# Kernel tuning notes

Hardware: AMD Instinct MI355X
Metric: run time of the kernel (lower is better)

## Reference

```python
import jax, jax.numpy as jnp
import numpy as np

N = 40000
E = 640000
IN_C = 128
HID = 256
HEADS = 8


def _gat(x, W, att_src, att_dst, bias, src, dst, num_nodes, heads, concat):
    # x: [N, Fin], W: [Fin, heads*C], att_*: [heads, C], bias: [out_dim]
    xp = (x @ W).reshape(num_nodes, heads, -1)          # [N, H, C]
    a_s = jnp.sum(xp * att_src, axis=-1)                # [N, H]
    a_d = jnp.sum(xp * att_dst, axis=-1)                # [N, H]
    e = jax.nn.leaky_relu(a_s[src] + a_d[dst], 0.2)     # [E, H]
    # per-destination-node softmax over incoming edges (self-loops guarantee >=1)
    m = jax.ops.segment_max(e, dst, num_segments=num_nodes)
    m = jnp.where(jnp.isfinite(m), m, 0.0)
    ex = jnp.exp(e - m[dst])
    denom = jax.ops.segment_sum(ex, dst, num_segments=num_nodes)
    alpha = ex / (denom[dst] + 1e-16)                   # [E, H]
    out = jax.ops.segment_sum(xp[src] * alpha[..., None], dst, num_segments=num_nodes)  # [N,H,C]
    out = out.reshape(num_nodes, -1) if concat else out.mean(axis=1)
    return out + bias


def setup_inputs() -> dict:
    key = jax.random.key(0)
    ks = jax.random.split(key, 16)
    C = HID // HEADS
    s = 0.05
    return {
        "x": jax.random.normal(ks[0], (N, IN_C), jnp.float32),
        "edge_index": jax.random.randint(ks[1], (2, E), 0, N, jnp.int32),
        "W0": jax.random.normal(ks[2], (IN_C, HEADS * C), jnp.float32) * s,
        "att_s0": jax.random.normal(ks[3], (HEADS, C), jnp.float32) * s,
        "att_d0": jax.random.normal(ks[4], (HEADS, C), jnp.float32) * s,
        "b0": jnp.zeros((HID,), jnp.float32),
        # BatchNorm(256)
        "gamma0": jnp.ones((HID,), jnp.float32),
        "beta0": jnp.zeros((HID,), jnp.float32),
        # skip projection Linear(128 -> 256)
        "W_skip": jax.random.normal(ks[5], (IN_C, HID), jnp.float32) * s,
        "b_skip": jnp.zeros((HID,), jnp.float32),
        # last layer: GATConv(256 -> 256, heads=1, concat=False)
        "W1": jax.random.normal(ks[6], (HID, HID), jnp.float32) * s,
        "att_s1": jax.random.normal(ks[7], (1, HID), jnp.float32) * s,
        "att_d1": jax.random.normal(ks[8], (1, HID), jnp.float32) * s,
        "b1": jnp.zeros((HID,), jnp.float32),
    }


def reference(x, edge_index, W0, att_s0, att_d0, b0, gamma0, beta0,
              W_skip, b_skip, W1, att_s1, att_d1, b1):
    loops = jnp.arange(N, dtype=edge_index.dtype)
    src = jnp.concatenate([edge_index[0], loops])
    dst = jnp.concatenate([edge_index[1], loops])
    # conv 0 (heads=8, concat)
    h = _gat(x, W0, att_s0, att_d0, b0, src, dst, N, HEADS, True)
    # BatchNorm (training-style batch stats, biased variance, eps=1e-5)
    mu = h.mean(axis=0)
    var = h.var(axis=0)
    h = (h - mu) / jnp.sqrt(var + 1e-5) * gamma0 + beta0
    h = jax.nn.elu(h)
    # dropout is identity in eval mode
    # residual: shapes differ (128 vs 256) -> skip_proj(x_initial) + h at i==0
    h = h + (x @ W_skip + b_skip)
    # conv 1 (heads=1, concat=False -> mean over single head)
    out = _gat(h, W1, att_s1, att_d1, b1, src, dst, N, 1, False)
    return out
```

## Files before the change

### kernel.cpp

```cpp
#include <hip/hip_runtime.h>
#include <hip/hip_bf16.h>

#define NN 40000
#define EE 640000
#define ET 680000
#define MPAD 40064
#define LOG2E 1.4426950408889634f

#define XN (MPAD * 128 / 4)
#define WN 131072
#define VN 512
#define PREP_TOTAL (XN + WN + VN + ET)

typedef __attribute__((ext_vector_type(8))) short short8;
typedef __attribute__((ext_vector_type(4))) float f32x4;

__device__ __forceinline__ float bf2f(unsigned u) {
    return __uint_as_float(u << 16);
}
__device__ __forceinline__ unsigned short f2bf(float f) {
    unsigned u = __float_as_uint(f);
    return (unsigned short)((u + 0x7FFFu + ((u >> 16) & 1u)) >> 16);
}
__device__ __forceinline__ unsigned pack2(float lo, float hi) {
    return ((unsigned)f2bf(lo)) | (((unsigned)f2bf(hi)) << 16);
}
__device__ __forceinline__ void unpack2(unsigned u, float& lo, float& hi) {
    lo = __uint_as_float(u << 16);
    hi = __uint_as_float(u & 0xffff0000u);
}

__global__ __launch_bounds__(256) void prep(
    const float* __restrict__ x, const float* __restrict__ W0,
    const float* __restrict__ Ws, const float* __restrict__ W1,
    const float* __restrict__ as1, const float* __restrict__ ad1,
    const int* __restrict__ ei,
    unsigned short* __restrict__ xb, unsigned short* __restrict__ Wtc,
    unsigned short* __restrict__ W1t, float* __restrict__ v,
    int* __restrict__ deg, int* __restrict__ erank)
{
    int i = blockIdx.x * 256 + threadIdx.x;
    if (i < XN) {
        int row = (i * 4) >> 7;
        ushort4 o;
        if (row < NN) {
            float4 val = ((const float4*)x)[i];
            o.x = f2bf(val.x); o.y = f2bf(val.y); o.z = f2bf(val.z); o.w = f2bf(val.w);
        } else { o.x = o.y = o.z = o.w = 0; }
        ((ushort4*)xb)[i] = o;
    } else if (i < XN + WN) {
        int j = i - XN;
        if (j < 32768) {
            int c = j >> 7, k = j & 127;
            Wtc[j] = f2bf(W0[(size_t)k * 256 + c]);
        } else if (j < 65536) {
            int jj = j - 32768;
            int c = jj >> 7, k = jj & 127;
            Wtc[j] = f2bf(Ws[(size_t)k * 256 + c]);
        } else {
            int jj = j - 65536;
            int c = jj >> 8, k = jj & 255;
            W1t[jj] = f2bf(W1[(size_t)k * 256 + c]);
        }
    } else if (i < XN + WN + VN) {
        int j = i - XN - WN;
        int k = j >> 1, which = j & 1;
        const float* att = which ? ad1 : as1;
        float sum = 0.f;
        for (int c = 0; c < 256; c++)
            sum += W1[(size_t)k * 256 + c] * att[c];
        v[j] = sum * LOG2E;
    } else {
        int e = i - XN - WN - VN;
        if (e < ET) {
            int d = (e < EE) ? ei[EE + e] : (e - EE);
            erank[e] = atomicAdd(&deg[d], 1);
        }
    }
}

__global__ __launch_bounds__(1024) void exscan(
    const int* __restrict__ deg, int* __restrict__ rowptr)
{
    __shared__ int wsum[16];
    __shared__ int carry_s;
    int tid = threadIdx.x, lane = tid & 63, wid = tid >> 6;
    if (tid == 0) carry_s = 0;
    __syncthreads();
    for (int base = 0; base < NN; base += 1024) {
        int i = base + tid;
        int val = (i < NN) ? deg[i] : 0;
        int sc = val;
        #pragma unroll
        for (int off = 1; off < 64; off <<= 1) {
            int t = __shfl_up(sc, off);
            if (lane >= off) sc += t;
        }
        if (lane == 63) wsum[wid] = sc;
        __syncthreads();
        if (wid == 0 && lane < 16) {
            int t = wsum[lane];
            #pragma unroll
            for (int off = 1; off < 16; off <<= 1) {
                int u = __shfl_up(t, off);
                if (lane >= off) t += u;
            }
            wsum[lane] = t;
        }
        __syncthreads();
        int carry = carry_s;
        int wpre = wid ? wsum[wid - 1] : 0;
        int excl = carry + wpre + sc - val;
        if (i < NN) rowptr[i] = excl;
        __syncthreads();
        if (tid == 0) carry_s = carry + wsum[15];
    }
    if (tid == 0) rowptr[NN] = carry_s;
}

__global__ __launch_bounds__(256) void csr_fill(
    const int* __restrict__ ei, const int* __restrict__ rowptr,
    const int* __restrict__ erank, int* __restrict__ adj)
{
    int e = blockIdx.x * blockDim.x + threadIdx.x;
    if (e >= ET) return;
    int s, d;
    if (e < EE) { s = ei[e]; d = ei[EE + e]; } else { s = d = e - EE; }
    adj[rowptr[d] + erank[e]] = s;
}

__global__ __launch_bounds__(256) void gemm0(
    const unsigned short* __restrict__ A, const unsigned short* __restrict__ Btc,
    unsigned short* __restrict__ C0, unsigned short* __restrict__ C1)
{
    __shared__ unsigned short As[128 * 64];
    const int K = 128;
    int tid = threadIdx.x;
    int rb = blockIdx.x * 128, cb = blockIdx.y * 128;
    int lane = tid & 63, wid = tid >> 6;
    int wm = (wid >> 1) * 64, wn = (wid & 1) * 64;
    int lr = lane & 15, lk = lane >> 4;
    f32x4 acc[4][4] = {};
    for (int kb = 0; kb < K; kb += 64) {
        #pragma unroll
        for (int i = 0; i < 4; i++) {
            int flat = tid + i * 256;
            int r = flat >> 3, c8 = flat & 7;
            int4 vv = *(const int4*)(A + (size_t)(rb + r) * K + kb + c8 * 8);
            *(int4*)(&As[r * 64 + ((c8 ^ (r & 7)) * 8)]) = vv;
        }
        __syncthreads();
        #pragma unroll
        for (int kk = 0; kk < 2; kk++) {
            int kbase = kb + kk * 32 + lk * 8;
            short8 bfr[4], afr[4];
            #pragma unroll
            for (int n = 0; n < 4; n++)
                bfr[n] = *(const short8*)(Btc + (size_t)(cb + wn + n * 16 + lr) * K + kbase);
            #pragma unroll
            for (int m = 0; m < 4; m++) {
                int row = wm + m * 16 + lr;
                int kchunk = kk * 4 + lk;
                afr[m] = *(const short8*)(&As[row * 64 + ((kchunk ^ (row & 7)) * 8)]);
            }
            #pragma unroll
            for (int m = 0; m < 4; m++)
                #pragma unroll
                for (int n = 0; n < 4; n++)
                    acc[m][n] = __builtin_amdgcn_mfma_f32_16x16x32_bf16(afr[m], bfr[n], acc[m][n], 0, 0, 0);
        }
        __syncthreads();
    }
    unsigned short* C = (cb < 256) ? C0 : C1;
    int cbase = cb & 255;
    #pragma unroll
    for (int m = 0; m < 4; m++)
        #pragma unroll
        for (int n = 0; n < 4; n++) {
            int col = cbase + wn + n * 16 + lr;
            #pragma unroll
            for (int j = 0; j < 4; j++) {
                int row = rb + wm + m * 16 + lk * 4 + j;
                C[(size_t)row * 256 + col] = f2bf(acc[m][n][j]);
            }
        }
}

__global__ __launch_bounds__(256) void gemm_bf16(
    const unsigned short* __restrict__ A, const unsigned short* __restrict__ Btc,
    unsigned short* __restrict__ C0, int K)
{
    __shared__ unsigned short As[128 * 64];
    int tid = threadIdx.x;
    int rb = blockIdx.x * 128, cb = blockIdx.y * 128;
    int lane = tid & 63, wid = tid >> 6;
    int wm = (wid >> 1) * 64, wn = (wid & 1) * 64;
    int lr = lane & 15, lk = lane >> 4;
    f32x4 acc[4][4] = {};
    for (int kb = 0; kb < K; kb += 64) {
        #pragma unroll
        for (int i = 0; i < 4; i++) {
            int flat = tid + i * 256;
            int r = flat >> 3, c8 = flat & 7;
            int4 vv = *(const int4*)(A + (size_t)(rb + r) * K + kb + c8 * 8);
            *(int4*)(&As[r * 64 + ((c8 ^ (r & 7)) * 8)]) = vv;
        }
        __syncthreads();
        #pragma unroll
        for (int kk = 0; kk < 2; kk++) {
            int kbase = kb + kk * 32 + lk * 8;
            short8 bfr[4], afr[4];
            #pragma unroll
            for (int n = 0; n < 4; n++)
                bfr[n] = *(const short8*)(Btc + (size_t)(cb + wn + n * 16 + lr) * K + kbase);
            #pragma unroll
            for (int m = 0; m < 4; m++) {
                int row = wm + m * 16 + lr;
                int kchunk = kk * 4 + lk;
                afr[m] = *(const short8*)(&As[row * 64 + ((kchunk ^ (row & 7)) * 8)]);
            }
            #pragma unroll
            for (int m = 0; m < 4; m++)
                #pragma unroll
                for (int n = 0; n < 4; n++)
                    acc[m][n] = __builtin_amdgcn_mfma_f32_16x16x32_bf16(afr[m], bfr[n], acc[m][n], 0, 0, 0);
        }
        __syncthreads();
    }
    #pragma unroll
    for (int m = 0; m < 4; m++)
        #pragma unroll
        for (int n = 0; n < 4; n++) {
            int col = cb + wn + n * 16 + lr;
            #pragma unroll
            for (int j = 0; j < 4; j++) {
                int row = rb + wm + m * 16 + lk * 4 + j;
                C0[(size_t)row * 256 + col] = f2bf(acc[m][n][j]);
            }
        }
}

__global__ __launch_bounds__(256) void attn_node0(
    const unsigned short* __restrict__ xp, const float* __restrict__ att_s,
    const float* __restrict__ att_d, float* __restrict__ a_s, float* __restrict__ a_d)
{
    int t = blockIdx.x * 256 + threadIdx.x;
    if (t >= NN * 8) return;
    int n = t >> 3, h = t & 7;
    const unsigned short* p = xp + (size_t)n * 256 + h * 32;
    float s = 0.f, dd = 0.f;
    #pragma unroll
    for (int i0 = 0; i0 < 32; i0 += 8) {
        uint4 raw = *(const uint4*)(p + i0);
        unsigned vals[4] = {raw.x, raw.y, raw.z, raw.w};
        #pragma unroll
        for (int q = 0; q < 4; q++) {
            float lo, hi;
            unpack2(vals[q], lo, hi);
            s  += lo * att_s[h * 32 + i0 + q * 2] + hi * att_s[h * 32 + i0 + q * 2 + 1];
            dd += lo * att_d[h * 32 + i0 + q * 2] + hi * att_d[h * 32 + i0 + q * 2 + 1];
        }
    }
    a_s[t] = s * LOG2E; a_d[t] = dd * LOG2E;
}

__global__ __launch_bounds__(256) void gather0(
    const int* __restrict__ adj, const int* __restrict__ rowptr,
    const unsigned short* __restrict__ xp, const float* __restrict__ a_s,
    const float* __restrict__ a_d, unsigned short* __restrict__ out0)
{
    int w = (blockIdx.x * 256 + threadIdx.x) >> 6;
    int lane = threadIdx.x & 63;
    if (w >= NN) return;
    int hl = lane & 31;
    int hw = lane >> 5;
    int h = hl >> 2;
    float ad = a_d[w * 8 + h];
    int p = rowptr[w], end = rowptr[w + 1];
    unsigned loff = (unsigned)hl * 16u;
    float a0=0,a1=0,a2=0,a3=0,a4=0,a5=0,a6=0,a7=0;
    float b0=0,b1=0,b2=0,b3=0,b4=0,b5=0,b6=0,b7=0;
    float den0 = 0.f, den1 = 0.f;
    float lo, hi;
    for (; p + 4 <= end; p += 4) {
        int sA = adj[p + hw];
        int sB = adj[p + 2 + hw];
        float eA = a_s[sA * 8 + h] + ad;
        float eB = a_s[sB * 8 + h] + ad;
        float wA = __builtin_amdgcn_exp2f(fmaxf(eA, 0.2f * eA));
        float wB = __builtin_amdgcn_exp2f(fmaxf(eB, 0.2f * eB));
        uint4 rA = *(const uint4*)((const char*)xp + ((unsigned)sA * 512u + loff));
        uint4 rB = *(const uint4*)((const char*)xp + ((unsigned)sB * 512u + loff));
        den0 += wA; den1 += wB;
        unpack2(rA.x, lo, hi); a0 += wA * lo; a1 += wA * hi;
        unpack2(rA.y, lo, hi); a2 += wA * lo; a3 += wA * hi;
        unpack2(rA.z, lo, hi); a4 += wA * lo; a5 += wA * hi;
        unpack2(rA.w, lo, hi); a6 += wA * lo; a7 += wA * hi;
        unpack2(rB.x, lo, hi); b0 += wB * lo; b1 += wB * hi;
        unpack2(rB.y, lo, hi); b2 += wB * lo; b3 += wB * hi;
        unpack2(rB.z, lo, hi); b4 += wB * lo; b5 += wB * hi;
        unpack2(rB.w, lo, hi); b6 += wB * lo; b7 += wB * hi;
    }
    for (; p + 2 <= end; p += 2) {
        int sA = adj[p + hw];
        float eA = a_s[sA * 8 + h] + ad;
        float wA = __builtin_amdgcn_exp2f(fmaxf(eA, 0.2f * eA));
        uint4 rA = *(const uint4*)((const char*)xp + ((unsigned)sA * 512u + loff));
        den0 += wA;
        unpack2(rA.x, lo, hi); a0 += wA * lo; a1 += wA * hi;
        unpack2(rA.y, lo, hi); a2 += wA * lo; a3 += wA * hi;
        unpack2(rA.z, lo, hi); a4 += wA * lo; a5 += wA * hi;
        unpack2(rA.w, lo, hi); a6 += wA * lo; a7 += wA * hi;
    }
    if (p < end) {
        int sA = adj[p];
        float eA = a_s[sA * 8 + h] + ad;
        float wA = hw ? 0.f : __builtin_amdgcn_exp2f(fmaxf(eA, 0.2f * eA));
        uint4 rA = *(const uint4*)((const char*)xp + ((unsigned)sA * 512u + loff));
        den0 += wA;
        unpack2(rA.x, lo, hi); a0 += wA * lo; a1 += wA * hi;
        unpack2(rA.y, lo, hi); a2 += wA * lo; a3 += wA * hi;
        unpack2(rA.z, lo, hi); a4 += wA * lo; a5 += wA * hi;
        unpack2(rA.w, lo, hi); a6 += wA * lo; a7 += wA * hi;
    }
    a0 += b0; a1 += b1; a2 += b2; a3 += b3;
    a4 += b4; a5 += b5; a6 += b6; a7 += b7;
    float den = den0 + den1;
    den += __shfl_xor(den, 32);
    a0 += __shfl_xor(a0, 32); a1 += __shfl_xor(a1, 32);
    a2 += __shfl_xor(a2, 32); a3 += __shfl_xor(a3, 32);
    a4 += __shfl_xor(a4, 32); a5 += __shfl_xor(a5, 32);
    a6 += __shfl_xor(a6, 32); a7 += __shfl_xor(a7, 32);
    if (hw == 0) {
        float inv = 1.f / (den + 1e-16f);
        uint4 o;
        o.x = pack2(a0 * inv, a1 * inv);
        o.y = pack2(a2 * inv, a3 * inv);
        o.z = pack2(a4 * inv, a5 * inv);
        o.w = pack2(a6 * inv, a7 * inv);
        *(uint4*)((char*)out0 + ((size_t)w * 512u + loff)) = o;
    }
}

__global__ __launch_bounds__(256) void bn_stats(
    const unsigned short* __restrict__ H, float* __restrict__ bnsum, float* __restrict__ bnsq)
{
    int c = threadIdx.x;
    int r0 = blockIdx.x * 64;
    float s = 0.f, sq = 0.f;
    for (int r = r0; r < r0 + 64; r++) {
        float val = bf2f(H[(size_t)r * 256 + c]);
        s += val; sq += val * val;
    }
    atomicAdd(&bnsum[c], s);
    atomicAdd(&bnsq[c], sq);
}

__global__ __launch_bounds__(256) void bn_elu_attn(
    const unsigned short* __restrict__ out0, unsigned short* __restrict__ hb,
    const float* __restrict__ bnsum, const float* __restrict__ bnsq,
    const float* __restrict__ gamma, const float* __restrict__ beta,
    const float* __restrict__ bskip, const float* __restrict__ v,
    float* __restrict__ a_s, float* __restrict__ a_d)
{
    int i = blockIdx.x * 256 + threadIdx.x;
    if (i >= MPAD * 32) return;
    int col0 = (i * 8) & 255;
    int row = i >> 5;
    uint4 hv = ((const uint4*)out0)[i];
    uint4 sv = ((const uint4*)hb)[i];
    float bn[8], sk[8];
    unpack2(hv.x, bn[0], bn[1]); unpack2(hv.y, bn[2], bn[3]);
    unpack2(hv.z, bn[4], bn[5]); unpack2(hv.w, bn[6], bn[7]);
    unpack2(sv.x, sk[0], sk[1]); unpack2(sv.y, sk[2], sk[3]);
    unpack2(sv.z, sk[4], sk[5]); unpack2(sv.w, sk[6], sk[7]);
    const float invN = 1.0f / (float)NN;
    float r[8];
    float ps = 0.f, pd = 0.f;
    #pragma unroll
    for (int q = 0; q < 8; q++) {
        int c = col0 + q;
        float mu = bnsum[c] * invN;
        float var = bnsq[c] * invN - mu * mu;
        float scl = rsqrtf(var + 1e-5f) * gamma[c];
        float b = (bn[q] - mu) * scl + beta[c];
        float el = b > 0.f ? b : (__expf(b) - 1.f);
        r[q] = el + sk[q] + bskip[c];
        float2 vv = *(const float2*)(v + c * 2);
        ps += r[q] * vv.x;
        pd += r[q] * vv.y;
    }
    uint4 o;
    o.x = pack2(r[0], r[1]); o.y = pack2(r[2], r[3]);
    o.z = pack2(r[4], r[5]); o.w = pack2(r[6], r[7]);
    ((uint4*)hb)[i] = o;
    #pragma unroll
    for (int off = 1; off < 32; off <<= 1) {
        ps += __shfl_xor(ps, off);
        pd += __shfl_xor(pd, off);
    }
    if ((threadIdx.x & 31) == 0 && row < NN) {
        a_s[row] = ps;
        a_d[row] = pd;
    }
}

__global__ __launch_bounds__(256) void gather1(
    const int* __restrict__ adj, const int* __restrict__ rowptr,
    const unsigned short* __restrict__ xp, const float* __restrict__ a_s,
    const float* __restrict__ a_d, const float* __restrict__ b1,
    float* __restrict__ out)
{
    int w = (blockIdx.x * 256 + threadIdx.x) >> 6;
    int lane = threadIdx.x & 63;
    if (w >= NN) return;
    int hl = lane & 31;
    int hw = lane >> 5;
    float ad = a_d[w];
    int p = rowptr[w], end = rowptr[w + 1];
    unsigned loff = (unsigned)hl * 16u;
    float a0=0,a1=0,a2=0,a3=0,a4=0,a5=0,a6=0,a7=0;
    float b0s=0,b1s=0,b2s=0,b3s=0,b4s=0,b5s=0,b6s=0,b7s=0;
    float den0 = 0.f, den1 = 0.f;
    float lo, hi;
    for (; p + 4 <= end; p += 4) {
        int sA = adj[p + hw];
        int sB = adj[p + 2 + hw];
        float eA = a_s[sA] + ad;
        float eB = a_s[sB] + ad;
        float wA = __builtin_amdgcn_exp2f(fmaxf(eA, 0.2f * eA));
        float wB = __builtin_amdgcn_exp2f(fmaxf(eB, 0.2f * eB));
        uint4 rA = *(const uint4*)((const char*)xp + ((unsigned)sA * 512u + loff));
        uint4 rB = *(const uint4*)((const char*)xp + ((unsigned)sB * 512u + loff));
        den0 += wA; den1 += wB;
        unpack2(rA.x, lo, hi); a0 += wA * lo; a1 += wA * hi;
        unpack2(rA.y, lo, hi); a2 += wA * lo; a3 += wA * hi;
        unpack2(rA.z, lo, hi); a4 += wA * lo; a5 += wA * hi;
        unpack2(rA.w, lo, hi); a6 += wA * lo; a7 += wA * hi;
        unpack2(rB.x, lo, hi); b0s += wB * lo; b1s += wB * hi;
        unpack2(rB.y, lo, hi); b2s += wB * lo; b3s += wB * hi;
        unpack2(rB.z, lo, hi); b4s += wB * lo; b5s += wB * hi;
        unpack2(rB.w, lo, hi); b6s += wB * lo; b7s += wB * hi;
    }
    for (; p + 2 <= end; p += 2) {
        int sA = adj[p + hw];
        float eA = a_s[sA] + ad;
        float wA = __builtin_amdgcn_exp2f(fmaxf(eA, 0.2f * eA));
        uint4 rA = *(const uint4*)((const char*)xp + ((unsigned)sA * 512u + loff));
        den0 += wA;
        unpack2(rA.x, lo, hi); a0 += wA * lo; a1 += wA * hi;
        unpack2(rA.y, lo, hi); a2 += wA * lo; a3 += wA * hi;
        unpack2(rA.z, lo, hi); a4 += wA * lo; a5 += wA * hi;
        unpack2(rA.w, lo, hi); a6 += wA * lo; a7 += wA * hi;
    }
    if (p < end) {
        int sA = adj[p];
        float eA = a_s[sA] + ad;
        float wA = hw ? 0.f : __builtin_amdgcn_exp2f(fmaxf(eA, 0.2f * eA));
        uint4 rA = *(const uint4*)((const char*)xp + ((unsigned)sA * 512u + loff));
        den0 += wA;
        unpack2(rA.x, lo, hi); a0 += wA * lo; a1 += wA * hi;
        unpack2(rA.y, lo, hi); a2 += wA * lo; a3 += wA * hi;
        unpack2(rA.z, lo, hi); a4 += wA * lo; a5 += wA * hi;
        unpack2(rA.w, lo, hi); a6 += wA * lo; a7 += wA * hi;
    }
    a0 += b0s; a1 += b1s; a2 += b2s; a3 += b3s;
    a4 += b4s; a5 += b5s; a6 += b6s; a7 += b7s;
    float den = den0 + den1;
    den += __shfl_xor(den, 32);
    a0 += __shfl_xor(a0, 32); a1 += __shfl_xor(a1, 32);
    a2 += __shfl_xor(a2, 32); a3 += __shfl_xor(a3, 32);
    a4 += __shfl_xor(a4, 32); a5 += __shfl_xor(a5, 32);
    a6 += __shfl_xor(a6, 32); a7 += __shfl_xor(a7, 32);
    if (hw == 0) {
        float inv = 1.f / (den + 1e-16f);
        const float* bb = b1 + hl * 8;
        float4 o0 = {a0 * inv + bb[0], a1 * inv + bb[1],
                     a2 * inv + bb[2], a3 * inv + bb[3]};
        float4 o1 = {a4 * inv + bb[4], a5 * inv + bb[5],
                     a6 * inv + bb[6], a7 * inv + bb[7]};
        float* orow = out + (size_t)w * 256 + hl * 8;
        *(float4*)(orow) = o0;
        *(float4*)(orow + 4) = o1;
    }
}

extern "C" void kernel_launch(void* const* d_in, const int* in_sizes, int n_in,
                              void* d_out, int out_size, void* d_ws, size_t ws_size,
                              hipStream_t stream)
{
    const float* x      = (const float*)d_in[0];
    const int*   ei     = (const int*)d_in[1];
    const float* W0     = (const float*)d_in[2];
    const float* att_s0 = (const float*)d_in[3];
    const float* att_d0 = (const float*)d_in[4];
    const float* gamma0 = (const float*)d_in[6];
    const float* beta0  = (const float*)d_in[7];
    const float* W_skip = (const float*)d_in[8];
    const float* b_skip = (const float*)d_in[9];
    const float* W1     = (const float*)d_in[10];
    const float* att_s1 = (const float*)d_in[11];
    const float* att_d1 = (const float*)d_in[12];
    const float* b1     = (const float*)d_in[13];
    float* out = (float*)d_out;

    char* p = (char*)d_ws;
    unsigned short* x_bf  = (unsigned short*)p; p += (size_t)MPAD * 128 * 2;
    unsigned short* xp_bf = (unsigned short*)p; p += (size_t)MPAD * 256 * 2;
    unsigned short* h_bf  = (unsigned short*)p; p += (size_t)MPAD * 256 * 2;
    unsigned short* out0b = (unsigned short*)p; p += (size_t)MPAD * 256 * 2;
    unsigned short* Wtc   = (unsigned short*)p; p += (size_t)512 * 128 * 2;
    unsigned short* W1t   = (unsigned short*)p; p += (size_t)256 * 256 * 2;
    float* v     = (float*)p; p += 512 * 4;
    float* a_s   = (float*)p; p += (size_t)NN * 8 * 4;
    float* a_d   = (float*)p; p += (size_t)NN * 8 * 4;
    int*   deg   = (int*)p;   p += (size_t)NN * 4;
    float* bnsum = (float*)p; p += 256 * 4;
    float* bnsq  = (float*)p; p += 256 * 4;
    int* rowptr = (int*)p; p += (size_t)(NN + 1) * 4;
    int* erank  = (int*)p; p += (size_t)ET * 4;
    int* adj    = (int*)p; p += (size_t)ET * 4;

    hipMemsetAsync(deg, 0, (size_t)(NN + 512) * 4, stream);
    hipMemsetAsync(out0b + (size_t)NN * 256, 0, (size_t)(MPAD - NN) * 256 * 2, stream);

    prep<<<(PREP_TOTAL + 255) / 256, 256, 0, stream>>>(
        x, W0, W_skip, W1, att_s1, att_d1, ei, x_bf, Wtc, W1t, v, deg, erank);

    exscan<<<1, 1024, 0, stream>>>(deg, rowptr);

    csr_fill<<<(ET + 255) / 256, 256, 0, stream>>>(ei, rowptr, erank, adj);

    dim3 gg0(MPAD / 128, 4);
    gemm0<<<gg0, 256, 0, stream>>>(x_bf, Wtc, xp_bf, h_bf);

    attn_node0<<<(NN * 8 + 255) / 256, 256, 0, stream>>>(xp_bf, att_s0, att_d0, a_s, a_d);

    gather0<<<(NN * 64 + 255) / 256, 256, 0, stream>>>(adj, rowptr, xp_bf, a_s, a_d, out0b);

    bn_stats<<<NN / 64, 256, 0, stream>>>(out0b, bnsum, bnsq);

    bn_elu_attn<<<(MPAD * 32 + 255) / 256, 256, 0, stream>>>(
        out0b, h_bf, bnsum, bnsq, gamma0, beta0, b_skip, v, a_s, a_d);

    dim3 gg1(MPAD / 128, 2);
    gemm_bf16<<<gg1, 256, 0, stream>>>(h_bf, W1t, xp_bf, 256);

    gather1<<<(NN * 64 + 255) / 256, 256, 0, stream>>>(adj, rowptr, xp_bf, a_s, a_d, b1, out);
}
```

Measured before the change: 288.6 us.

## Fold layer-0 attention vectors into W0 and merge attention with CSR fill

Precomputes u = W0·att (per head, scaled by log2e) in the prep kernel, so the layer-0 attention logits come straight from x in bf16 (128-wide dot products) rather than from the GEMM output. This removes the dependency on gemm0, which lets the attention computation join the CSR fill kernel and removes one launch. The tradeoff is more arithmetic per node (128 vs 32 elements per head), and the logits now differ slightly in rounding because they skip the bf16-rounded xp.

```diff
diff --git a/kernel.cpp b/kernel.cpp
--- a/kernel.cpp
+++ b/kernel.cpp
@@ -10,7 +10,11 @@
 #define XN (MPAD * 128 / 4)
 #define WN 131072
 #define VN 512
-#define PREP_TOTAL (XN + WN + VN + ET)
+#define UN 2048
+#define PREP_TOTAL (XN + WN + VN + UN + ET)
+
+#define FB ((ET + 255) / 256)
+#define AB ((NN * 8 + 255) / 256)
 
 typedef __attribute__((ext_vector_type(8))) short short8;
 typedef __attribute__((ext_vector_type(4))) float f32x4;
@@ -33,10 +37,11 @@
 __global__ __launch_bounds__(256) void prep(
     const float* __restrict__ x, const float* __restrict__ W0,
     const float* __restrict__ Ws, const float* __restrict__ W1,
+    const float* __restrict__ as0, const float* __restrict__ ad0,
     const float* __restrict__ as1, const float* __restrict__ ad1,
     const int* __restrict__ ei,
     unsigned short* __restrict__ xb, unsigned short* __restrict__ Wtc,
-    unsigned short* __restrict__ W1t, float* __restrict__ v,
+    unsigned short* __restrict__ W1t, float* __restrict__ v, float* __restrict__ u,
     int* __restrict__ deg, int* __restrict__ erank)
 {
     int i = blockIdx.x * 256 + threadIdx.x;
@@ -70,8 +75,18 @@
         for (int c = 0; c < 256; c++)
             sum += W1[(size_t)k * 256 + c] * att[c];
         v[j] = sum * LOG2E;
+    } else if (i < XN + WN + VN + UN) {
+        int j = i - XN - WN - VN;
+        int k = j >> 4, jj = j & 15;
+        int h = jj & 7;
+        const float* att = (jj < 8) ? as0 : ad0;
+        float sum = 0.f;
+        #pragma unroll
+        for (int c = 0; c < 32; c++)
+            sum += W0[(size_t)k * 256 + h * 32 + c] * att[h * 32 + c];
+        u[j] = sum * LOG2E;
     } else {
-        int e = i - XN - WN - VN;
+        int e = i - XN - WN - VN - UN;
         if (e < ET) {
             int d = (e < EE) ? ei[EE + e] : (e - EE);
             erank[e] = atomicAdd(&deg[d], 1);
@@ -102,8 +117,8 @@
             int t = wsum[lane];
             #pragma unroll
             for (int off = 1; off < 16; off <<= 1) {
-                int u = __shfl_up(t, off);
-                if (lane >= off) t += u;
+                int uu = __shfl_up(t, off);
+                if (lane >= off) t += uu;
             }
             wsum[lane] = t;
         }
@@ -118,15 +133,40 @@
     if (tid == 0) rowptr[NN] = carry_s;
 }
 
-__global__ __launch_bounds__(256) void csr_fill(
+__global__ __launch_bounds__(256) void fill_attn0(
     const int* __restrict__ ei, const int* __restrict__ rowptr,
-    const int* __restrict__ erank, int* __restrict__ adj)
-{
-    int e = blockIdx.x * blockDim.x + threadIdx.x;
-    if (e >= ET) return;
-    int s, d;
-    if (e < EE) { s = ei[e]; d = ei[EE + e]; } else { s = d = e - EE; }
-    adj[rowptr[d] + erank[e]] = s;
+    const int* __restrict__ erank, int* __restrict__ adj,
+    const unsigned short* __restrict__ xb, const float* __restrict__ u,
+    float* __restrict__ a_s, float* __restrict__ a_d)
+{
+    int tid = threadIdx.x;
+    if (blockIdx.x < FB) {
+        int e = blockIdx.x * 256 + tid;
+        if (e >= ET) return;
+        int s, d;
+        if (e < EE) { s = ei[e]; d = ei[EE + e]; } else { s = d = e - EE; }
+        adj[rowptr[d] + erank[e]] = s;
+        return;
+    }
+    int t = (blockIdx.x - FB) * 256 + tid;
+    if (t >= NN * 8) return;
+    int n = t >> 3, h = t & 7;
+    const uint4* xr = (const uint4*)(xb + (size_t)n * 128);
+    float s = 0.f, dd = 0.f;
+    #pragma unroll
+    for (int q = 0; q < 16; q++) {
+        uint4 raw = xr[q];
+        unsigned vals[4] = {raw.x, raw.y, raw.z, raw.w};
+        #pragma unroll
+        for (int r = 0; r < 4; r++) {
+            float lo, hi;
+            unpack2(vals[r], lo, hi);
+            int c = q * 8 + r * 2;
+            s  += lo * u[c * 16 + h]     + hi * u[(c + 1) * 16 + h];
+            dd += lo * u[c * 16 + 8 + h] + hi * u[(c + 1) * 16 + 8 + h];
+        }
+    }
+    a_s[t] = s; a_d[t] = dd;
 }
 
 __global__ __launch_bounds__(256) void gemm0(
@@ -238,30 +278,6 @@
                 C0[(size_t)row * 256 + col] = f2bf(acc[m][n][j]);
             }
         }
-}
-
-__global__ __launch_bounds__(256) void attn_node0(
-    const unsigned short* __restrict__ xp, const float* __restrict__ att_s,
-    const float* __restrict__ att_d, float* __restrict__ a_s, float* __restrict__ a_d)
-{
-    int t = blockIdx.x * 256 + threadIdx.x;
-    if (t >= NN * 8) return;
-    int n = t >> 3, h = t & 7;
-    const unsigned short* p = xp + (size_t)n * 256 + h * 32;
-    float s = 0.f, dd = 0.f;
-    #pragma unroll
-    for (int i0 = 0; i0 < 32; i0 += 8) {
-        uint4 raw = *(const uint4*)(p + i0);
-        unsigned vals[4] = {raw.x, raw.y, raw.z, raw.w};
-        #pragma unroll
-        for (int q = 0; q < 4; q++) {
-            float lo, hi;
-            unpack2(vals[q], lo, hi);
-            s  += lo * att_s[h * 32 + i0 + q * 2] + hi * att_s[h * 32 + i0 + q * 2 + 1];
-            dd += lo * att_d[h * 32 + i0 + q * 2] + hi * att_d[h * 32 + i0 + q * 2 + 1];
-        }
-    }
-    a_s[t] = s * LOG2E; a_d[t] = dd * LOG2E;
 }
 
 __global__ __launch_bounds__(256) void gather0(
@@ -512,6 +528,7 @@
     unsigned short* Wtc   = (unsigned short*)p; p += (size_t)512 * 128 * 2;
     unsigned short* W1t   = (unsigned short*)p; p += (size_t)256 * 256 * 2;
     float* v     = (float*)p; p += 512 * 4;
+    float* u     = (float*)p; p += 2048 * 4;
     float* a_s   = (float*)p; p += (size_t)NN * 8 * 4;
     float* a_d   = (float*)p; p += (size_t)NN * 8 * 4;
     int*   deg   = (int*)p;   p += (size_t)NN * 4;
@@ -525,17 +542,16 @@
     hipMemsetAsync(out0b + (size_t)NN * 256, 0, (size_t)(MPAD - NN) * 256 * 2, stream);
 
     prep<<<(PREP_TOTAL + 255) / 256, 256, 0, stream>>>(
-        x, W0, W_skip, W1, att_s1, att_d1, ei, x_bf, Wtc, W1t, v, deg, erank);
+        x, W0, W_skip, W1, att_s0, att_d0, att_s1, att_d1, ei,
+        x_bf, Wtc, W1t, v, u, deg, erank);
 
     exscan<<<1, 1024, 0, stream>>>(deg, rowptr);
 
-    csr_fill<<<(ET + 255) / 256, 256, 0, stream>>>(ei, rowptr, erank, adj);
+    fill_attn0<<<FB + AB, 256, 0, stream>>>(ei, rowptr, erank, adj, x_bf, u, a_s, a_d);
 
     dim3 gg0(MPAD / 128, 4);
     gemm0<<<gg0, 256, 0, stream>>>(x_bf, Wtc, xp_bf, h_bf);
 
-    attn_node0<<<(NN * 8 + 255) / 256, 256, 0, stream>>>(xp_bf, att_s0, att_d0, a_s, a_d);
-
     gather0<<<(NN * 64 + 255) / 256, 256, 0, stream>>>(adj, rowptr, xp_bf, a_s, a_d, out0b);
 
     bn_stats<<<NN / 64, 256, 0, stream>>>(out0b, bnsum, bnsq);
```

Result: no change. 288.8 us (median of 2 runs) (+0.1%).
